# Performance work log

Hardware: AMD Instinct MI355X
Metric: run time of the kernel (lower is better)

Reference implementation:

```python
import jax, jax.numpy as jnp
import numpy as np

N_NODES = 200000
N_EDGES = 2000000
B = 1024
SEQ = 1000
EMB = 128
VOC = 26  # num_features_xt + 1
BN_EPS = 1e-5


def setup_inputs() -> dict:
    key = jax.random.key(0)
    ks = jax.random.split(key, 40)
    f32 = jnp.float32
    def nrm(k, shp, s=0.05):
        return jax.random.normal(k, shp, dtype=f32) * s
    inp = {}
    inp['x'] = jax.random.normal(ks[0], (N_NODES, 78), dtype=f32)
    inp['edge_index'] = jax.random.randint(ks[1], (2, N_EDGES), 0, N_NODES, dtype=jnp.int32)
    inp['batch'] = jnp.sort(jax.random.randint(ks[2], (N_NODES,), 0, B, dtype=jnp.int32))
    inp['target'] = jax.random.randint(ks[3], (B, SEQ), 0, VOC, dtype=jnp.int32)
    # GIN layer 1 (78 -> 32 -> 32)
    inp['W1a'] = nrm(ks[4], (78, 32)); inp['b1a'] = jnp.zeros((32,), f32)
    inp['W2a'] = nrm(ks[5], (32, 32)); inp['b2a'] = jnp.zeros((32,), f32)
    inp['g1'] = jnp.ones((32,), f32); inp['be1'] = jnp.zeros((32,), f32)
    # GIN layers 2-5 stacked
    inp['Ws1'] = nrm(ks[6], (4, 32, 32)); inp['bs1'] = jnp.zeros((4, 32), f32)
    inp['Ws2'] = nrm(ks[7], (4, 32, 32)); inp['bs2'] = jnp.zeros((4, 32), f32)
    inp['gs'] = jnp.ones((4, 32), f32); inp['bes'] = jnp.zeros((4, 32), f32)
    # drug head
    inp['fc1xd_W'] = nrm(ks[8], (32, 128)); inp['fc1xd_b'] = jnp.zeros((128,), f32)
    # protein branch
    inp['emb'] = nrm(ks[9], (VOC, EMB), 1.0)
    inp['convW'] = nrm(ks[10], (32, SEQ, 8))  # Conv1d(1000, 32, k=8): (O, I, K)
    inp['convb'] = jnp.zeros((32,), f32)
    inp['fcxt_W'] = nrm(ks[11], (32 * 121, 128)); inp['fcxt_b'] = jnp.zeros((128,), f32)
    # joint head
    inp['fc1_W'] = nrm(ks[12], (256, 1024)); inp['fc1_b'] = jnp.zeros((1024,), f32)
    inp['fc2_W'] = nrm(ks[13], (1024, 256)); inp['fc2_b'] = jnp.zeros((256,), f32)
    inp['out_W'] = nrm(ks[14], (256, 1)); inp['out_b'] = jnp.zeros((1,), f32)
    return inp


def _bn(h, g, b):
    m = h.mean(axis=0)
    v = h.var(axis=0)
    return (h - m) * jax.lax.rsqrt(v + BN_EPS) * g + b


def _gin(x, src, dst, W1, b1, W2, b2):
    # GIN aggregation (eps=0): (1+eps)*x + sum_{j->i} x_j, then 2-layer MLP
    agg = jax.ops.segment_sum(x[src], dst, num_segments=x.shape[0]) + x
    return jnp.maximum(agg @ W1 + b1, 0.0) @ W2 + b2


def reference(x, edge_index, batch, target, W1a, b1a, W2a, b2a, g1, be1,
              Ws1, bs1, Ws2, bs2, gs, bes, fc1xd_W, fc1xd_b, emb, convW, convb,
              fcxt_W, fcxt_b, fc1_W, fc1_b, fc2_W, fc2_b, out_W, out_b):
    relu = jax.nn.relu
    src, dst = edge_index[0], edge_index[1]
    h = _bn(relu(_gin(x, src, dst, W1a, b1a, W2a, b2a)), g1, be1)
    for i in range(4):
        h = _bn(relu(_gin(h, src, dst, Ws1[i], bs1[i], Ws2[i], bs2[i])), gs[i], bes[i])
    nb = target.shape[0]
    pooled = jax.ops.segment_sum(h, batch, num_segments=nb)  # [B, 32]
    xd = relu(pooled @ fc1xd_W + fc1xd_b)  # dropout: identity at eval
    # protein branch: embedding [B, 1000, 128] -> Conv1d over C=1000, L=128
    xe = emb[target]
    conv = jax.lax.conv_general_dilated(xe, convW, (1,), 'VALID',
                                        dimension_numbers=('NCH', 'OIH', 'NCH'))
    conv = conv + convb[None, :, None]  # [B, 32, 121]
    xt = conv.reshape(nb, 32 * 121) @ fcxt_W + fcxt_b
    xc = jnp.concatenate([xd, xt], axis=1)
    xc = relu(xc @ fc1_W + fc1_b)
    xc = relu(xc @ fc2_W + fc2_b)
    return xc @ out_W + out_b
```

## Files before the change

### kernel.cpp

```cpp
#include <hip/hip_runtime.h>

#define N_NODES 200000
#define N_EDGES 2000000
#define BATCH   1024
#define SEQ     1000
#define EMBD    128
#define VOC     26
#define BN_EPS  1e-5f
#define NB      128
#define NBUK    1563
#define CAP     1664
#define STG     8192
#define BPT     7



__global__ __launch_bounds__(256, 1) void k_bscatter(const int* __restrict__ ei,
                                                     int* __restrict__ gcnt,
                                                     unsigned int* __restrict__ epk) {
    __shared__ int lcnt[NBUK];
    __shared__ int lpos[NBUK];
    __shared__ int sbase[NBUK];
    __shared__ int ssum[256];
    __shared__ int2 stage[STG];
    int tid = threadIdx.x;
    int e0 = blockIdx.x * STG;
    int m = min(STG, N_EDGES - e0);
    for (int i = tid; i < NBUK; i += 256) lcnt[i] = 0;
    __syncthreads();
    for (int i = tid; i < m; i += 256) {
        int d = ei[N_EDGES + e0 + i];
        atomicAdd(&lcnt[d >> 7], 1);
    }
    __syncthreads();
    int v[BPT]; int s0 = 0; int bb = tid * BPT;
#pragma unroll
    for (int k = 0; k < BPT; k++) {
        int idx = bb + k;
        v[k] = (idx < NBUK) ? lcnt[idx] : 0;
        s0 += v[k];
    }
    ssum[tid] = s0;
    __syncthreads();
    for (int off = 1; off < 256; off <<= 1) {
        int x = (tid >= off) ? ssum[tid - off] : 0;
        __syncthreads();
        ssum[tid] += x;
        __syncthreads();
    }
    int run = ssum[tid] - s0;
#pragma unroll
    for (int k = 0; k < BPT; k++) {
        int idx = bb + k;
        if (idx < NBUK) { lpos[idx] = run; run += v[k]; }
    }
    __syncthreads();
    for (int i = tid; i < NBUK; i += 256) {
        int c = lcnt[i];
        if (c > 0) {
            int gb = atomicAdd(&gcnt[i], c);
            sbase[i] = gb - lpos[i];
        }
    }
    __syncthreads();
    for (int i = tid; i < m; i += 256) {
        int s = ei[e0 + i];
        int d = ei[N_EDGES + e0 + i];
        int p = atomicAdd(&lpos[d >> 7], 1);
        stage[p] = make_int2(s, d);
    }
    __syncthreads();
    for (int i = tid; i < m; i += 256) {
        int2 ed = stage[i];
        int b = ed.y >> 7;
        int slot = sbase[b] + i;
        if (slot < CAP)
            epk[(size_t)b * CAP + slot] = ((unsigned int)ed.x << 8) | (unsigned int)(ed.y & 127);
    }
}

__global__ __launch_bounds__(256, 8) void k_bsort(const int* __restrict__ gcnt,
                                                  unsigned int* __restrict__ epk,
                                                  int* __restrict__ deg) {
    __shared__ unsigned int stg[CAP];
    __shared__ unsigned int srt[CAP];
    __shared__ int cnt[NB];
    __shared__ int pos[NB];
    int b = blockIdx.x, tid = threadIdx.x;
    int fill = min(gcnt[b], CAP);
    unsigned int* slab = epk + (size_t)b * CAP;
    for (int i = tid; i < fill; i += 256) stg[i] = slab[i];
    if (tid < NB) cnt[tid] = 0;
    __syncthreads();
    for (int i = tid; i < fill; i += 256) atomicAdd(&cnt[stg[i] & (NB - 1)], 1);
    __syncthreads();
    if (tid < NB) { pos[tid] = cnt[tid]; deg[b * NB + tid] = cnt[tid]; }
    __syncthreads();
    for (int off = 1; off < NB; off <<= 1) {
        int x = (tid < NB && tid >= off) ? pos[tid - off] : 0;
        __syncthreads();
        if (tid < NB) pos[tid] += x;
        __syncthreads();
    }
    if (tid < NB) cnt[tid] = pos[tid] - cnt[tid];
    __syncthreads();
    for (int i = tid; i < fill; i += 256) {
        int p = atomicAdd(&cnt[stg[i] & (NB - 1)], 1);
        srt[p] = stg[i];
    }
    __syncthreads();
    for (int i = tid; i < fill; i += 256) slab[i] = srt[i];
}


__global__ __launch_bounds__(128) void k_proj78(const float* __restrict__ x,
                                                const float* __restrict__ W,
                                                float* __restrict__ y) {
    __shared__ __align__(16) float xs[128 * 78];
    __shared__ __align__(16) float ws[78 * 32];
    int tid = threadIdx.x;
    int base = blockIdx.x * 128;
    for (int i = tid; i < 78 * 32; i += 128) ws[i] = W[i];
    int cnt = min(128, N_NODES - base);
    for (int i = tid; i < cnt * 78; i += 128) xs[i] = x[(size_t)base * 78 + i];
    __syncthreads();
    int n = base + tid;
    if (tid >= cnt) return;
    float acc[32];
#pragma unroll
    for (int j = 0; j < 32; j++) acc[j] = 0.f;
    const float* xr = &xs[tid * 78];
    for (int c = 0; c < 78; c++) {
        float xv = xr[c];
        const float4* w4 = (const float4*)&ws[c * 32];
#pragma unroll
        for (int j4 = 0; j4 < 8; j4++) {
            float4 w = w4[j4];
            acc[j4 * 4 + 0] += xv * w.x; acc[j4 * 4 + 1] += xv * w.y;
            acc[j4 * 4 + 2] += xv * w.z; acc[j4 * 4 + 3] += xv * w.w;
        }
    }
    float4* yo = (float4*)&y[(size_t)n * 32];
#pragma unroll
    for (int j4 = 0; j4 < 8; j4++)
        yo[j4] = make_float4(acc[j4*4], acc[j4*4+1], acc[j4*4+2], acc[j4*4+3]);
}

template <bool FOLD>
__global__ __launch_bounds__(256, 5) void k_gmlp(const float* __restrict__ hin,
                                                 const int* __restrict__ gcnt,
                                                 const unsigned int* __restrict__ epk,
                                                 const int* __restrict__ deg,
                                                 const float* __restrict__ stats,
                                                 const float* __restrict__ g,
                                                 const float* __restrict__ be,
                                                 const float* __restrict__ W1,
                                                 const float* __restrict__ b1,
                                                 const float* __restrict__ W2,
                                                 const float* __restrict__ b2,
                                                 float* __restrict__ h,
                                                 float* __restrict__ statsOut) {
    __shared__ __align__(16) float ts[129 * 33];
    __shared__ __align__(16) float w2s[1024];
    __shared__ __align__(16) unsigned int es[CAP];
    __shared__ float b1s[32], b2s[32], as_[32], cs_[32], cv[32];
    int tid = threadIdx.x, base = blockIdx.x * NB;
    for (int i = tid; i < 1024; i += 256) w2s[i] = W2[i];
    if (tid < 32) { b1s[tid] = b1[tid]; b2s[tid] = b2[tid]; }
    int cnt = min(NB, N_NODES - base);
    int fill = min(gcnt[blockIdx.x], CAP);
    int pfill = (fill + 127) & ~127;
    int dg = 0;
    if (FOLD && tid < cnt) dg = deg[base + tid];
    for (int i = tid; i < fill; i += 256) es[i] = epk[(size_t)blockIdx.x * CAP + i];
    for (int i = fill + tid; i < pfill; i += 256) es[i] = 128u;
    for (int i = tid; i < cnt * 32; i += 256) ts[(i >> 5) * 33 + (i & 31)] = hin[(size_t)base * 32 + i];
    __syncthreads();
    {
        int hw = tid >> 5, c = tid & 31;
        for (int se = hw * 16; se < pfill; se += 128) {
            float rr[16]; int dd[16];
#pragma unroll
            for (int k = 0; k < 16; k++) {
                unsigned int p = es[se + k];
                rr[k] = hin[(size_t)(p >> 8) * 32 + c];
                dd[k] = (int)(p & 255u);
            }
            float acc = rr[0]; int cur = dd[0];
#pragma unroll
            for (int k = 1; k < 16; k++) {
                if (dd[k] == cur) acc += rr[k];
                else { atomicAdd(&ts[cur * 33 + c], acc); acc = rr[k]; cur = dd[k]; }
            }
            if (cur < 128) atomicAdd(&ts[cur * 33 + c], acc);
        }
    }
    __syncthreads();
    float* wc  = (float*)es;
    float* spq = ((float*)es) + 1024;
    if constexpr (FOLD) {
        if (tid < 32) {
            float inv_n = 1.f / (float)N_NODES;
            float m = stats[tid] * inv_n;
            float var = stats[32 + tid] * inv_n - m * m;
            float a = g[tid] * rsqrtf(var + BN_EPS);
            as_[tid] = a;
            cs_[tid] = be[tid] - m * a;
        }
        __syncthreads();
        for (int i = tid; i < 1024; i += 256) wc[i] = as_[i >> 5] * W1[i];
        if (tid < 32) {
            float s = 0.f;
            for (int k = 0; k < 32; k++) s += cs_[k] * W1[k * 32 + tid];
            cv[tid] = s;
        }
        __syncthreads();
    }
    float t[32];
    if (tid < cnt) {
        float v[32];
        if constexpr (FOLD) {
            float dgf = (float)(dg + 1);
#pragma unroll
            for (int j = 0; j < 32; j++) v[j] = b1s[j] + dgf * cv[j];
            for (int c = 0; c < 32; c++) {
                float av = ts[tid * 33 + c];
                const float4* w4 = (const float4*)&wc[c * 32];
#pragma unroll
                for (int j4 = 0; j4 < 8; j4++) {
                    float4 w = w4[j4];
                    v[j4*4+0] += av * w.x; v[j4*4+1] += av * w.y;
                    v[j4*4+2] += av * w.z; v[j4*4+3] += av * w.w;
                }
            }
        } else {
#pragma unroll
            for (int c = 0; c < 32; c++) v[c] = ts[tid * 33 + c] + b1s[c];
        }
        float acc[32];
#pragma unroll
        for (int j = 0; j < 32; j++) acc[j] = b2s[j];
        for (int c = 0; c < 32; c++) {
            float zv = fmaxf(v[c], 0.f);
            const float4* w4 = (const float4*)&w2s[c * 32];
#pragma unroll
            for (int j4 = 0; j4 < 8; j4++) {
                float4 w = w4[j4];
                acc[j4*4+0] += zv * w.x; acc[j4*4+1] += zv * w.y;
                acc[j4*4+2] += zv * w.z; acc[j4*4+3] += zv * w.w;
            }
        }
#pragma unroll
        for (int j = 0; j < 32; j++) t[j] = fmaxf(acc[j], 0.f);
    } else {
#pragma unroll
        for (int j = 0; j < 32; j++) t[j] = 0.f;
    }
    __syncthreads();
    if (tid < NB) {
#pragma unroll
        for (int c = 0; c < 32; c++) ts[tid * 33 + c] = t[c];
    }
    __syncthreads();
    {
        int c = tid & 31, gg = tid >> 5;
        float s = 0.f, q = 0.f;
        for (int r = gg * 16; r < gg * 16 + 16; r++) { float vv = ts[r * 33 + c]; s += vv; q += vv * vv; }
        spq[gg * 32 + c] = s; spq[256 + gg * 32 + c] = q;
    }
    __syncthreads();
    if (tid < 32) {
        float s = 0.f, q = 0.f;
#pragma unroll
        for (int gg = 0; gg < 8; gg++) { s += spq[gg * 32 + tid]; q += spq[256 + gg * 32 + tid]; }
        atomicAdd(&statsOut[tid], s);
        atomicAdd(&statsOut[32 + tid], q);
    }
    for (int i = tid; i < cnt * 32; i += 256) h[(size_t)base * 32 + i] = ts[(i >> 5) * 33 + (i & 31)];
}

__device__ __forceinline__ int lbound(const int* __restrict__ b, int val) {
    int lo = 0, hi = N_NODES;
    while (lo < hi) { int mid = (lo + hi) >> 1; if (b[mid] < val) lo = mid + 1; else hi = mid; }
    return lo;
}

__global__ __launch_bounds__(256) void k_pool(const float* __restrict__ h,
                                              const int* __restrict__ batch,
                                              const float* __restrict__ stats,
                                              const float* __restrict__ gw,
                                              const float* __restrict__ be,
                                              float* __restrict__ pooled) {
    __shared__ float sp[8][32];
    int g = blockIdx.x;
    int start = lbound(batch, g), end = lbound(batch, g + 1);
    int c = threadIdx.x & 31, gg = threadIdx.x >> 5;
    float acc = 0.f;
    for (int r = start + gg; r < end; r += 8) acc += h[(size_t)r * 32 + c];
    sp[gg][c] = acc;
    __syncthreads();
    if (threadIdx.x < 32) {
        int j = threadIdx.x;
        float s = 0.f;
#pragma unroll
        for (int k = 0; k < 8; k++) s += sp[k][j];
        float inv_n = 1.f / (float)N_NODES;
        float m = stats[j] * inv_n;
        float var = stats[32 + j] * inv_n - m * m;
        float a = gw[j] * rsqrtf(var + BN_EPS);
        float cc = be[j] - m * a;
        pooled[g * 32 + j] = a * s + cc * (float)(end - start);
    }
}

__global__ __launch_bounds__(256) void k_xd(const float* __restrict__ pooled,
                                            const float* __restrict__ W,
                                            const float* __restrict__ b,
                                            float* __restrict__ xc) {
    int t = blockIdx.x * 256 + threadIdx.x;
    int row = t >> 7, col = t & 127;
    if (row >= BATCH) return;
    float acc = b[col];
    for (int k = 0; k < 32; k++) acc += pooled[row * 32 + k] * W[k * 128 + col];
    xc[row * 256 + col] = fmaxf(acc, 0.f);
}


__global__ __launch_bounds__(256) void k_trw(const float* __restrict__ convW,
                                             float* __restrict__ Wt) {
    int t = blockIdx.x * 256 + threadIdx.x;
    if (t >= 32 * SEQ * 8) return;
    int o = t / (SEQ * 8), r = t % (SEQ * 8), i = r >> 3, k = r & 7;
    Wt[i * 256 + o * 8 + k] = convW[t];
}

__global__ __launch_bounds__(256) void k_prot1(const int* __restrict__ target,
                                               const float* __restrict__ Wt,
                                               float* __restrict__ Sg) {
    __shared__ int tv[SEQ];
    __shared__ int pos_[SEQ];
    __shared__ int off_[VOC + 1];
    __shared__ int cur_[VOC];
    int tid = threadIdx.x, b = blockIdx.x;
    for (int i = tid; i < SEQ; i += 256) tv[i] = target[(size_t)b * SEQ + i];
    if (tid < VOC + 1) off_[tid] = 0;
    __syncthreads();
    for (int i = tid; i < SEQ; i += 256) atomicAdd(&off_[tv[i] + 1], 1);
    __syncthreads();
    if (tid == 0) for (int v = 1; v <= VOC; v++) off_[v] += off_[v - 1];
    __syncthreads();
    if (tid < VOC) cur_[tid] = off_[tid];
    __syncthreads();
    for (int i = tid; i < SEQ; i += 256) {
        int p = atomicAdd(&cur_[tv[i]], 1);
        pos_[p] = i;
    }
    __syncthreads();
    for (int v = 0; v < VOC; v++) {
        int e0 = off_[v], e1 = off_[v + 1];
        float a0 = 0.f, a1 = 0.f, a2 = 0.f, a3 = 0.f, a4 = 0.f, a5 = 0.f, a6 = 0.f, a7 = 0.f;
        int k = e0;
        for (; k + 8 <= e1; k += 8) {
            a0 += Wt[(size_t)pos_[k + 0] * 256 + tid];
            a1 += Wt[(size_t)pos_[k + 1] * 256 + tid];
            a2 += Wt[(size_t)pos_[k + 2] * 256 + tid];
            a3 += Wt[(size_t)pos_[k + 3] * 256 + tid];
            a4 += Wt[(size_t)pos_[k + 4] * 256 + tid];
            a5 += Wt[(size_t)pos_[k + 5] * 256 + tid];
            a6 += Wt[(size_t)pos_[k + 6] * 256 + tid];
            a7 += Wt[(size_t)pos_[k + 7] * 256 + tid];
        }
        for (; k < e1; k++) a0 += Wt[(size_t)pos_[k] * 256 + tid];
        Sg[((size_t)b * VOC + v) * 256 + tid] = ((a0 + a1) + (a2 + a3)) + ((a4 + a5) + (a6 + a7));
    }
}

__global__ __launch_bounds__(256, 4) void k_prot2(const float* __restrict__ Sg,
                                                  const float* __restrict__ emb,
                                                  const float* __restrict__ convb,
                                                  float* __restrict__ conv) {
    __shared__ __align__(16) float S[VOC * 256];
    __shared__ __align__(16) float embs[VOC * EMBD];
    int tid = threadIdx.x, b = blockIdx.x;
    for (int i = tid; i < VOC * 256; i += 256) S[i] = Sg[(size_t)b * (VOC * 256) + i];
    for (int i = tid; i < VOC * EMBD; i += 256) embs[i] = emb[i];
    __syncthreads();
    int og = tid >> 6, lt = tid & 63;
    bool has2 = (lt < 57);
    float acc0[8], acc1[8];
#pragma unroll
    for (int oi = 0; oi < 8; oi++) {
        float bb = convb[og * 8 + oi];
        acc0[oi] = bb; acc1[oi] = bb;
    }
    for (int v = 0; v < VOC; v++) {
        float er0[8], er1[8];
#pragma unroll
        for (int k = 0; k < 8; k++) er0[k] = embs[v * EMBD + lt + k];
#pragma unroll
        for (int k = 0; k < 8; k++) er1[k] = has2 ? embs[v * EMBD + lt + 64 + k] : 0.f;
        const float* sv = &S[v * 256 + og * 64];
#pragma unroll
        for (int oi = 0; oi < 8; oi++) {
#pragma unroll
            for (int k = 0; k < 8; k++) {
                float s = sv[oi * 8 + k];
                acc0[oi] += s * er0[k];
                acc1[oi] += s * er1[k];
            }
        }
    }
#pragma unroll
    for (int oi = 0; oi < 8; oi++) {
        int o = og * 8 + oi;
        conv[((size_t)b * 32 + o) * 121 + lt] = acc0[oi];
        if (has2) conv[((size_t)b * 32 + o) * 121 + lt + 64] = acc1[oi];
    }
}


__global__ __launch_bounds__(256) void k_init_bias(float* __restrict__ C, int ldc, int coff,
                                                   const float* __restrict__ bias, int nb) {
    int t = blockIdx.x * 256 + threadIdx.x;
    int row = t / nb, col = t % nb;
    if (row >= BATCH) return;
    C[row * ldc + coff + col] = bias[col];
}

template <int ROWS, bool ATOMIC, bool RELU>
__global__ __launch_bounds__(256, 3) void k_gemm(const float* __restrict__ A, int lda,
                                                 const float* __restrict__ W, int ldw,
                                                 const float* __restrict__ bias,
                                                 float* __restrict__ C, int ldc, int coff,
                                                 int mtc, int ntc, int klen) {
    constexpr int P  = ROWS + 4;
    constexpr int HR = ROWS / 2;
    constexpr int TPR = 256 / ROWS;
    __shared__ __align__(16) float As[64 * P];
    __shared__ __align__(16) float Ws[64 * 128];
    int bid = blockIdx.x;
    int mt = bid % mtc, nt = (bid / mtc) % ntc, ks = bid / (mtc * ntc);
    int row0 = mt * ROWS, col0 = nt * 128, k0 = ks * klen;
    int tid = threadIdx.x;
    int j = tid & 127, rh = tid >> 7;
    float acc[HR];
#pragma unroll
    for (int m = 0; m < HR; m++) acc[m] = (ATOMIC || bias == nullptr) ? 0.f : bias[col0 + j];
    int lr = tid / TPR, lk = tid % TPR;
    for (int kc = 0; kc < klen; kc += 64) {
        int cc = min(64, klen - kc);
        __syncthreads();
        for (int kk = lk; kk < cc; kk += TPR)
            As[kk * P + lr] = A[(size_t)(row0 + lr) * lda + k0 + kc + kk];
        for (int i = tid; i < cc * 32; i += 256) {
            int r = i >> 5, c4 = (i & 31) << 2;
            *(float4*)&Ws[r * 128 + c4] =
                *(const float4*)&W[(size_t)(k0 + kc + r) * ldw + col0 + c4];
        }
        __syncthreads();
#pragma unroll 4
        for (int kk = 0; kk < cc; kk++) {
            float w = Ws[kk * 128 + j];
            const float4* a4 = (const float4*)&As[kk * P + rh * HR];
#pragma unroll
            for (int m4 = 0; m4 < HR / 4; m4++) {
                float4 a = a4[m4];
                acc[m4*4+0] += a.x * w; acc[m4*4+1] += a.y * w;
                acc[m4*4+2] += a.z * w; acc[m4*4+3] += a.w * w;
            }
        }
    }
#pragma unroll
    for (int m = 0; m < HR; m++) {
        int row = row0 + rh * HR + m;
        float* p = &C[(size_t)row * ldc + coff + col0 + j];
        if (ATOMIC) atomicAdd(p, acc[m]);
        else { float v = acc[m]; if (RELU) v = fmaxf(v, 0.f); *p = v; }
    }
}

__global__ __launch_bounds__(256) void k_out(const float* __restrict__ xc2,
                                             const float* __restrict__ W,
                                             const float* __restrict__ b,
                                             float* __restrict__ out) {
    int gt = blockIdx.x * 256 + threadIdx.x;
    int wid = gt >> 6, lane = gt & 63;
    if (wid >= BATCH) return;
    float4 xv = ((const float4*)&xc2[(size_t)wid * 256])[lane];
    float4 wv = ((const float4*)W)[lane];
    float s = fmaxf(xv.x, 0.f) * wv.x + fmaxf(xv.y, 0.f) * wv.y +
              fmaxf(xv.z, 0.f) * wv.z + fmaxf(xv.w, 0.f) * wv.w;
    for (int off = 32; off; off >>= 1) s += __shfl_down(s, off, 64);
    if (lane == 0) out[wid] = s + b[0];
}


extern "C" void kernel_launch(void* const* d_in, const int* in_sizes, int n_in,
                              void* d_out, int out_size, void* d_ws, size_t ws_size,
                              hipStream_t stream) {
    const float* x      = (const float*)d_in[0];
    const int*   ei     = (const int*)d_in[1];
    const int*   batch  = (const int*)d_in[2];
    const int*   target = (const int*)d_in[3];
    const float* W1a = (const float*)d_in[4];
    const float* b1a = (const float*)d_in[5];
    const float* W2a = (const float*)d_in[6];
    const float* b2a = (const float*)d_in[7];
    const float* g1  = (const float*)d_in[8];
    const float* be1 = (const float*)d_in[9];
    const float* Ws1 = (const float*)d_in[10];
    const float* bs1 = (const float*)d_in[11];
    const float* Ws2 = (const float*)d_in[12];
    const float* bs2 = (const float*)d_in[13];
    const float* gs  = (const float*)d_in[14];
    const float* bes = (const float*)d_in[15];
    const float* fc1xd_W = (const float*)d_in[16];
    const float* fc1xd_b = (const float*)d_in[17];
    const float* emb   = (const float*)d_in[18];
    const float* convW = (const float*)d_in[19];
    const float* convb = (const float*)d_in[20];
    const float* fcxt_W = (const float*)d_in[21];
    const float* fcxt_b = (const float*)d_in[22];
    const float* fc1_W = (const float*)d_in[23];
    const float* fc1_b = (const float*)d_in[24];
    const float* fc2_W = (const float*)d_in[25];
    const float* fc2_b = (const float*)d_in[26];
    const float* out_W = (const float*)d_in[27];
    const float* out_b = (const float*)d_in[28];
    float* out = (float*)d_out;

    char* ws = (char*)d_ws;
    size_t off = 0;
    auto alloc = [&](size_t bytes) { char* p = ws + off; off += (bytes + 4095) & ~(size_t)4095; return p; };
    float* y    = (float*)alloc((size_t)N_NODES * 32 * 4);
    float* h    = (float*)alloc((size_t)N_NODES * 32 * 4);
    unsigned int* epk = (unsigned int*)alloc((size_t)NBUK * CAP * 4);
    int* gcnt = (int*)alloc((size_t)NBUK * 4);
    float* stats  = (float*)alloc(5 * 64 * 4);
    float* pooled = (float*)alloc(BATCH * 32 * 4);
    float* xc  = (float*)alloc(BATCH * 256 * 4);
    float* xc1 = (float*)alloc(BATCH * 1024 * 4);
    float* xc2 = (float*)alloc(BATCH * 256 * 4);
    float* Wt  = (float*)alloc(SEQ * 256 * 4);
    int* deg  = (int*)alloc((size_t)NBUK * NB * 4);
    float* Sg   = h;
    float* conv = y;

    hipMemsetAsync(stats, 0, 5 * 64 * 4, stream);
    hipMemsetAsync(gcnt, 0, (size_t)NBUK * 4, stream);

    const int PROJ78_G = (N_NODES + 127) / 128;
    const int PART_G   = (N_EDGES + STG - 1) / STG;

    k_bscatter<<<PART_G, 256, 0, stream>>>(ei, gcnt, epk);
    k_bsort<<<NBUK, 256, 0, stream>>>(gcnt, epk, deg);

    k_proj78<<<PROJ78_G, 128, 0, stream>>>(x, W1a, y);
    k_gmlp<false><<<NBUK, 256, 0, stream>>>(y, gcnt, epk, deg, nullptr, nullptr, nullptr,
                                            nullptr, b1a, W2a, b2a, h, stats);
    float* hin = h; float* hout = y;
    for (int i = 0; i < 4; i++) {
        const float* gg = (i == 0) ? g1 : gs + (i - 1) * 32;
        const float* bb = (i == 0) ? be1 : bes + (i - 1) * 32;
        k_gmlp<true><<<NBUK, 256, 0, stream>>>(hin, gcnt, epk, deg, stats + i * 64, gg, bb,
                                               Ws1 + i * 1024, bs1 + i * 32, Ws2 + i * 1024,
                                               bs2 + i * 32, hout, stats + (i + 1) * 64);
        float* tmp = hin; hin = hout; hout = tmp;
    }
    k_pool<<<BATCH, 256, 0, stream>>>(hin, batch, stats + 4 * 64, gs + 3 * 32, bes + 3 * 32, pooled);
    k_xd<<<(BATCH * 128) / 256, 256, 0, stream>>>(pooled, fc1xd_W, fc1xd_b, xc);
    k_trw<<<(32 * SEQ * 8) / 256, 256, 0, stream>>>(convW, Wt);
    k_prot1<<<BATCH, 256, 0, stream>>>(target, Wt, Sg);
    k_prot2<<<BATCH, 256, 0, stream>>>(Sg, emb, convb, conv);
    k_init_bias<<<(BATCH * 128) / 256, 256, 0, stream>>>(xc, 256, 128, fcxt_b, 128);
    k_gemm<32, true, false><<<32 * 1 * 16, 256, 0, stream>>>(conv, 3872, fcxt_W, 128, nullptr,
                                                             xc, 256, 128, 32, 1, 242);
    k_gemm<32, false, true><<<32 * 8 * 1, 256, 0, stream>>>(xc, 256, fc1_W, 1024, fc1_b,
                                                            xc1, 1024, 0, 32, 8, 256);
    k_init_bias<<<(BATCH * 256) / 256, 256, 0, stream>>>(xc2, 256, 0, fc2_b, 256);
    k_gemm<32, true, false><<<32 * 2 * 4, 256, 0, stream>>>(xc1, 1024, fc2_W, 256, nullptr,
                                                            xc2, 256, 0, 32, 2, 256);
    k_out<<<(BATCH * 64) / 256, 256, 0, stream>>>(xc2, out_W, out_b, out);
}
```

Before: 1.084 ms.

## Shrink GIN MLP shared memory to raise occupancy, chunk edge staging

Reduces the k_gmlp LDS footprint by staging the edge slab in two smaller chunks through a shared buffer and by reading W1/W2 straight from global memory (uniform, cache-resident) instead of copying them to LDS. The BN scale is now applied per input channel in the matmul rather than folded into a scaled weight copy. Launch bounds rise to allow more resident blocks per CU, and the bucket-scatter kernel halves its staging buffer to allow two blocks. The aim is to hide gather latency through higher occupancy, at the cost of extra barriers and global/scalar-cache weight loads inside the inner loops.

```diff
diff --git a/kernel.cpp b/kernel.cpp
--- a/kernel.cpp
+++ b/kernel.cpp
@@ -10,12 +10,14 @@
 #define NB      128
 #define NBUK    1563
 #define CAP     1664
-#define STG     8192
+#define CH0     896
+#define CH1     768
+#define STG     4096
 #define BPT     7
 
 
 
-__global__ __launch_bounds__(256, 1) void k_bscatter(const int* __restrict__ ei,
+__global__ __launch_bounds__(256, 2) void k_bscatter(const int* __restrict__ ei,
                                                      int* __restrict__ gcnt,
                                                      unsigned int* __restrict__ epk) {
     __shared__ int lcnt[NBUK];
@@ -147,7 +149,7 @@
 }
 
 template <bool FOLD>
-__global__ __launch_bounds__(256, 5) void k_gmlp(const float* __restrict__ hin,
+__global__ __launch_bounds__(256, 7) void k_gmlp(const float* __restrict__ hin,
                                                  const int* __restrict__ gcnt,
                                                  const unsigned int* __restrict__ epk,
                                                  const int* __restrict__ deg,
@@ -161,43 +163,14 @@
                                                  float* __restrict__ h,
                                                  float* __restrict__ statsOut) {
     __shared__ __align__(16) float ts[129 * 33];
-    __shared__ __align__(16) float w2s[1024];
-    __shared__ __align__(16) unsigned int es[CAP];
+    __shared__ __align__(16) unsigned int es[CH0];
     __shared__ float b1s[32], b2s[32], as_[32], cs_[32], cv[32];
     int tid = threadIdx.x, base = blockIdx.x * NB;
-    for (int i = tid; i < 1024; i += 256) w2s[i] = W2[i];
     if (tid < 32) { b1s[tid] = b1[tid]; b2s[tid] = b2[tid]; }
     int cnt = min(NB, N_NODES - base);
     int fill = min(gcnt[blockIdx.x], CAP);
-    int pfill = (fill + 127) & ~127;
     int dg = 0;
     if (FOLD && tid < cnt) dg = deg[base + tid];
-    for (int i = tid; i < fill; i += 256) es[i] = epk[(size_t)blockIdx.x * CAP + i];
-    for (int i = fill + tid; i < pfill; i += 256) es[i] = 128u;
-    for (int i = tid; i < cnt * 32; i += 256) ts[(i >> 5) * 33 + (i & 31)] = hin[(size_t)base * 32 + i];
-    __syncthreads();
-    {
-        int hw = tid >> 5, c = tid & 31;
-        for (int se = hw * 16; se < pfill; se += 128) {
-            float rr[16]; int dd[16];
-#pragma unroll
-            for (int k = 0; k < 16; k++) {
-                unsigned int p = es[se + k];
-                rr[k] = hin[(size_t)(p >> 8) * 32 + c];
-                dd[k] = (int)(p & 255u);
-            }
-            float acc = rr[0]; int cur = dd[0];
-#pragma unroll
-            for (int k = 1; k < 16; k++) {
-                if (dd[k] == cur) acc += rr[k];
-                else { atomicAdd(&ts[cur * 33 + c], acc); acc = rr[k]; cur = dd[k]; }
-            }
-            if (cur < 128) atomicAdd(&ts[cur * 33 + c], acc);
-        }
-    }
-    __syncthreads();
-    float* wc  = (float*)es;
-    float* spq = ((float*)es) + 1024;
     if constexpr (FOLD) {
         if (tid < 32) {
             float inv_n = 1.f / (float)N_NODES;
@@ -207,15 +180,49 @@
             as_[tid] = a;
             cs_[tid] = be[tid] - m * a;
         }
-        __syncthreads();
-        for (int i = tid; i < 1024; i += 256) wc[i] = as_[i >> 5] * W1[i];
+    }
+    for (int i = tid; i < cnt * 32; i += 256) ts[(i >> 5) * 33 + (i & 31)] = hin[(size_t)base * 32 + i];
+    if constexpr (FOLD) {
+        __syncthreads();
         if (tid < 32) {
             float s = 0.f;
             for (int k = 0; k < 32; k++) s += cs_[k] * W1[k * 32 + tid];
             cv[tid] = s;
         }
-        __syncthreads();
-    }
+    }
+    {
+        int hw = tid >> 5, c = tid & 31;
+        const unsigned int* slab = epk + (size_t)blockIdx.x * CAP;
+#pragma unroll
+        for (int ch = 0; ch < 2; ch++) {
+            int cbase = ch ? CH0 : 0;
+            int clen  = ch ? CH1 : CH0;
+            __syncthreads();
+            for (int i = tid; i < clen; i += 256) {
+                int gi = cbase + i;
+                es[i] = (gi < fill) ? slab[gi] : 128u;
+            }
+            __syncthreads();
+            for (int se = hw * 16; se < clen; se += 128) {
+                float rr[16]; int dd[16];
+#pragma unroll
+                for (int k = 0; k < 16; k++) {
+                    unsigned int p = es[se + k];
+                    rr[k] = hin[(size_t)(p >> 8) * 32 + c];
+                    dd[k] = (int)(p & 255u);
+                }
+                float acc = rr[0]; int cur = dd[0];
+#pragma unroll
+                for (int k = 1; k < 16; k++) {
+                    if (dd[k] == cur) acc += rr[k];
+                    else { atomicAdd(&ts[cur * 33 + c], acc); acc = rr[k]; cur = dd[k]; }
+                }
+                if (cur < 128) atomicAdd(&ts[cur * 33 + c], acc);
+            }
+        }
+    }
+    __syncthreads();
+    float* spq = (float*)es;
     float t[32];
     if (tid < cnt) {
         float v[32];
@@ -224,13 +231,13 @@
 #pragma unroll
             for (int j = 0; j < 32; j++) v[j] = b1s[j] + dgf * cv[j];
             for (int c = 0; c < 32; c++) {
-                float av = ts[tid * 33 + c];
-                const float4* w4 = (const float4*)&wc[c * 32];
+                float avs = ts[tid * 33 + c] * as_[c];
+                const float4* w4 = (const float4*)&W1[c * 32];
 #pragma unroll
                 for (int j4 = 0; j4 < 8; j4++) {
                     float4 w = w4[j4];
-                    v[j4*4+0] += av * w.x; v[j4*4+1] += av * w.y;
-                    v[j4*4+2] += av * w.z; v[j4*4+3] += av * w.w;
+                    v[j4*4+0] += avs * w.x; v[j4*4+1] += avs * w.y;
+                    v[j4*4+2] += avs * w.z; v[j4*4+3] += avs * w.w;
                 }
             }
         } else {
@@ -242,7 +249,7 @@
         for (int j = 0; j < 32; j++) acc[j] = b2s[j];
         for (int c = 0; c < 32; c++) {
             float zv = fmaxf(v[c], 0.f);
-            const float4* w4 = (const float4*)&w2s[c * 32];
+            const float4* w4 = (const float4*)&W2[c * 32];
 #pragma unroll
             for (int j4 = 0; j4 < 8; j4++) {
                 float4 w = w4[j4];
```

Result: faster. 1.016 ms (-6.3%).
